# Kernel optimization log

Hardware: AMD Instinct MI355X
Metric: run time of the kernel (lower is better)

The kernel has to match this reference:

```python
import math
import jax, jax.numpy as jnp
import numpy as np

N_HEADS = 16


def setup_inputs() -> dict:
    key = jax.random.key(0)
    k1, k2 = jax.random.split(key)
    qkv = jax.random.normal(k1, (2, 3072, 2048), dtype=jnp.float32)
    mask = jax.random.randint(k2, (2, 1, 2048), 0, 2).astype(jnp.bool_)
    return {"qkv": qkv, "mask": mask}


def reference(qkv, mask):
    bs, width, length = qkv.shape
    ch = width // (3 * N_HEADS)
    q, k, v = jnp.split(qkv, 3, axis=1)  # each [bs, H*C, T]
    scale = 1.0 / math.sqrt(math.sqrt(ch))  # applied to both q and k
    q = (q * scale).reshape(bs * N_HEADS, ch, length)
    k = (k * scale).reshape(bs * N_HEADS, ch, length)
    # [B*H, T, T] scores
    weight = jnp.einsum('bct,bcs->bts', q, k)
    # mask: [bs, 1, T] bool, True = valid token
    inv = ~mask[:, 0, :]                      # [bs, T]
    pad = inv[:, None, :] | inv[:, :, None]   # [bs, T, T]
    pad = jnp.broadcast_to(pad[:, None], (bs, N_HEADS, length, length))
    pad = pad.reshape(bs * N_HEADS, length, length)
    weight = jnp.where(pad, jnp.finfo(weight.dtype).min, weight)
    weight = jax.nn.softmax(weight.astype(jnp.float32), axis=-1).astype(qkv.dtype)
    a = jnp.einsum('bts,bcs->bct', weight, v.reshape(bs * N_HEADS, ch, length))
    return a.reshape(bs, N_HEADS * ch, length)
```

## Files before the change

kernel.cpp:

```cpp
#include <hip/hip_runtime.h>
#include <float.h>


typedef __attribute__((ext_vector_type(8))) short bf16x8;
typedef __attribute__((ext_vector_type(4))) float f32x4;

#define TSEQ 2048
#define QT_OFF 0L
#define KF_OFF 4194304L
#define VF_OFF 8388608L

#if __has_builtin(__builtin_amdgcn_exp2f)
#define EXPFN(x) __builtin_amdgcn_exp2f(x)
#define SM_SCALE (0.125f * 1.44269504088896f)
#else
#define EXPFN(x) __expf(x)
#define SM_SCALE 0.125f
#endif

__device__ inline short f2bf(float x) {
    union { float f; unsigned u; } un; un.f = x;
    unsigned r = un.u + 0x7fffu + ((un.u >> 16) & 1u);
    return (short)(r >> 16);
}

__device__ inline unsigned pkbf(float a, float b) {
    unsigned au = __float_as_uint(a) + 0x8000u;
    unsigned bu = __float_as_uint(b) + 0x8000u;
    return __builtin_amdgcn_perm(bu, au, 0x07060302u);
}

__global__ __launch_bounds__(256) void prep_kernel(
    const float* __restrict__ qkv, short* __restrict__ ws)
{
    const int tid = threadIdx.x;
    const int job = blockIdx.x;
    if (job < 2048) {
        __shared__ float Ls[64 * 65];
        const int which = job & 1;
        const int rest  = job >> 1;
        const int bh = rest & 31, tt = rest >> 5;
        const int b = bh >> 4, h = bh & 15;
        const float* src = qkv + (long)b * 6291456 + ((long)(which * 1024 + h * 64)) * TSEQ + tt * 64;
        #pragma unroll
        for (int ch = 0; ch < 4; ++ch) {
            int idx = tid + ch * 256;
            int c = idx >> 4, tch = idx & 15;
            float4 v = *(const float4*)(src + (long)c * TSEQ + tch * 4);
            float* L = &Ls[c * 65 + tch * 4];
            L[0] = v.x; L[1] = v.y; L[2] = v.z; L[3] = v.w;
        }
        __syncthreads();
        if (which == 0) {
            short* dst = ws + QT_OFF + ((long)bh * TSEQ + tt * 64) * 64;
            #pragma unroll
            for (int ch = 0; ch < 2; ++ch) {
                int idx = tid + ch * 256;
                int t = idx >> 3, cch = idx & 7;
                bf16x8 o;
                #pragma unroll
                for (int j = 0; j < 8; ++j)
                    o[j] = f2bf(Ls[(cch * 8 + j) * 65 + t] * SM_SCALE);
                *(bf16x8*)(dst + (long)t * 64 + cch * 8) = o;
            }
        } else {
            short* dst = ws + KF_OFF + (long)(bh * 32 + tt) * 4096;
            #pragma unroll
            for (int ch = 0; ch < 2; ++ch) {
                int u = tid + ch * 256;
                int f = u >> 6, lane = u & 63;
                int q = lane >> 4, l15 = lane & 15;
                int hf = f & 1, ns = f >> 1;
                bf16x8 o;
                #pragma unroll
                for (int j = 0; j < 8; ++j)
                    o[j] = f2bf(Ls[(hf * 32 + q * 8 + j) * 65 + ns * 16 + l15]);
                *(bf16x8*)(dst + f * 512 + lane * 8) = o;
            }
        }
    } else {
        const int v = job - 2048;
        const int head = v >> 5, it = v & 31;
        const int b = head >> 4, h = head & 15;
        short* dst = ws + VF_OFF + (long)(head * 32 + it) * 4096;
        #pragma unroll
        for (int ch = 0; ch < 2; ++ch) {
            int u = tid * 2 + ch;
            int f = u >> 6, lane = u & 63;
            int q = lane >> 4, l15 = lane & 15;
            int hf = f & 1, nc = f >> 1;
            const float* src = qkv + (long)b * 6291456
                + ((long)(2048 + h * 64 + nc * 16 + l15)) * TSEQ
                + it * 64 + hf * 32 + q * 8;
            float4 a  = *(const float4*)src;
            float4 c4 = *(const float4*)(src + 4);
            bf16x8 o;
            o[0] = f2bf(a.x);  o[1] = f2bf(a.y);  o[2] = f2bf(a.z);  o[3] = f2bf(a.w);
            o[4] = f2bf(c4.x); o[5] = f2bf(c4.y); o[6] = f2bf(c4.z); o[7] = f2bf(c4.w);
            *(bf16x8*)(dst + f * 512 + lane * 8) = o;
        }
    }
}

__global__ __launch_bounds__(512, 2) void attn_kernel(
    const short* __restrict__ ws, const int* __restrict__ mask,
    float* __restrict__ out)
{
    __shared__ __align__(16) char smem[66560];
    short* Ps  = (short*)smem;
    float* mbf = (float*)(smem + 32768);
    float* Os  = (float*)smem;

    const int tid  = threadIdx.x;
    const int lane = tid & 63, wid = tid >> 6;
    const int l15  = lane & 15, quad = lane >> 4;

    const int blk  = blockIdx.x;
    const int head = blk & 31;
    const int qt   = blk >> 5;
    const int b    = head >> 4, h = head & 15;
    const int t0   = qt * 256;

    const short* QT = ws + QT_OFF + (long)head * 131072;
    const short* KF = ws + KF_OFF + (long)head * 131072;
    const short* VF = ws + VF_OFF + (long)head * 131072;
    const long obase = ((long)b * 1024 + h * 64) * TSEQ;

    for (int i = tid; i < TSEQ; i += 512)
        mbf[i] = (mask[b * TSEQ + i] != 0) ? 0.0f : -1e30f;
    __syncthreads();

    bf16x8 qb[2][2];
    #pragma unroll
    for (int nt = 0; nt < 2; ++nt)
        #pragma unroll
        for (int hf = 0; hf < 2; ++hf)
            qb[nt][hf] = *(const bf16x8*)(QT +
                (long)(t0 + wid * 32 + nt * 16 + l15) * 64 + quad * 8 + hf * 32);
    bool qv[2];
    #pragma unroll
    for (int nt = 0; nt < 2; ++nt)
        qv[nt] = (mbf[t0 + wid * 32 + nt * 16 + l15] != 0.0f);

    float l_s[2] = {0.0f, 0.0f};
    f32x4 Oacc[2][4];
    #pragma unroll
    for (int mt = 0; mt < 2; ++mt)
        #pragma unroll
        for (int nc = 0; nc < 4; ++nc)
            #pragma unroll
            for (int r = 0; r < 4; ++r) Oacc[mt][nc][r] = 0.0f;

    short* Pw = Ps + wid * 2048;

    bf16x8 kc[8];
    #pragma unroll
    for (int f = 0; f < 8; ++f)
        kc[f] = *(const bf16x8*)(KF + (long)f * 512 + lane * 8);

    for (int it = 0; it < 32; ++it) {
        const int itn = (it + 1) & 31;

        bf16x8 vf[8];
        #pragma unroll
        for (int f = 0; f < 8; ++f)
            vf[f] = *(const bf16x8*)(VF + ((long)it * 8 + f) * 512 + lane * 8);
        bf16x8 kn[8];
        #pragma unroll
        for (int f = 0; f < 8; ++f)
            kn[f] = *(const bf16x8*)(KF + ((long)itn * 8 + f) * 512 + lane * 8);

        f32x4 bias[4];
        #pragma unroll
        for (int ns = 0; ns < 4; ++ns)
            bias[ns] = *(const f32x4*)&mbf[it * 64 + ns * 16 + quad * 4];

        f32x4 Sacc[4][2];
        #pragma unroll
        for (int ns = 0; ns < 4; ++ns)
            #pragma unroll
            for (int nt = 0; nt < 2; ++nt) {
                Sacc[ns][nt] = __builtin_amdgcn_mfma_f32_16x16x32_bf16(
                    kc[ns * 2 + 0], qb[nt][0], bias[ns], 0, 0, 0);
                Sacc[ns][nt] = __builtin_amdgcn_mfma_f32_16x16x32_bf16(
                    kc[ns * 2 + 1], qb[nt][1], Sacc[ns][nt], 0, 0, 0);
            }

        #pragma unroll
        for (int nt = 0; nt < 2; ++nt) {
            const int row = nt * 16 + l15;
            const int sw  = (row & 7) ^ ((row & 8) >> 1);
            float ls = 0.0f;
            #pragma unroll
            for (int ns = 0; ns < 4; ++ns) {
                float pv[4];
                #pragma unroll
                for (int r = 0; r < 4; ++r) {
                    float e = EXPFN(Sacc[ns][nt][r]);
                    pv[r] = qv[nt] ? 1.0f : e;
                    ls += pv[r];
                }
                const int cbp = (ns * 2 + (quad >> 1)) ^ sw;
                uint2 pk;
                pk.x = pkbf(pv[0], pv[1]);
                pk.y = pkbf(pv[2], pv[3]);
                *(uint2*)&Pw[row * 64 + cbp * 8 + (quad & 1) * 4] = pk;
            }
            ls += __shfl_xor(ls, 16);
            ls += __shfl_xor(ls, 32);
            l_s[nt] += ls;
        }

        bf16x8 pa[2][2];
        #pragma unroll
        for (int mt = 0; mt < 2; ++mt) {
            const int row = mt * 16 + l15;
            const int sw  = (row & 7) ^ ((row & 8) >> 1);
            #pragma unroll
            for (int hf = 0; hf < 2; ++hf)
                pa[mt][hf] = *(const bf16x8*)&Pw[row * 64 + ((quad + 4 * hf) ^ sw) * 8];
        }
        #pragma unroll
        for (int hf = 0; hf < 2; ++hf)
            #pragma unroll
            for (int nc = 0; nc < 4; ++nc)
                #pragma unroll
                for (int mt = 0; mt < 2; ++mt)
                    Oacc[mt][nc] = __builtin_amdgcn_mfma_f32_16x16x32_bf16(
                        pa[mt][hf], vf[nc * 2 + hf], Oacc[mt][nc], 0, 0, 0);

        #pragma unroll
        for (int f = 0; f < 8; ++f) kc[f] = kn[f];
    }

    __syncthreads();
    float inv[2];
    #pragma unroll
    for (int nt = 0; nt < 2; ++nt) inv[nt] = 1.0f / l_s[nt];
    float iw[2][4];
    #pragma unroll
    for (int mt = 0; mt < 2; ++mt)
        #pragma unroll
        for (int r = 0; r < 4; ++r)
            iw[mt][r] = __shfl(inv[mt], 4 * quad + r);
    #pragma unroll
    for (int mt = 0; mt < 2; ++mt)
        #pragma unroll
        for (int nc = 0; nc < 4; ++nc) {
            float4 o;
            o.x = Oacc[mt][nc][0] * iw[mt][0];
            o.y = Oacc[mt][nc][1] * iw[mt][1];
            o.z = Oacc[mt][nc][2] * iw[mt][2];
            o.w = Oacc[mt][nc][3] * iw[mt][3];
            *(float4*)&Os[(nc * 16 + l15) * 260 + wid * 32 + mt * 16 + quad * 4] = o;
        }
    __syncthreads();
    #pragma unroll
    for (int ch = 0; ch < 8; ++ch) {
        int idx = tid + ch * 512;
        int c = idx >> 6, tch = idx & 63;
        *(float4*)(out + obase + (long)c * TSEQ + t0 + tch * 4) =
            *(const float4*)&Os[c * 260 + tch * 4];
    }
}

extern "C" void kernel_launch(void* const* d_in, const int* in_sizes, int n_in,
                              void* d_out, int out_size, void* d_ws, size_t ws_size,
                              hipStream_t stream) {
    const float* qkv  = (const float*)d_in[0];
    const int*   mask = (const int*)d_in[1];
    float*       out  = (float*)d_out;
    short*       ws   = (short*)d_ws;
    prep_kernel<<<dim3(3072), dim3(256), 0, stream>>>(qkv, ws);
    attn_kernel<<<dim3(256), dim3(512), 0, stream>>>(ws, mask, out);
}
```

Measured before the change: 143.2 us.

## Stage K/V tiles through double-buffered LDS via direct global-to-LDS loads

The attention kernel now loads K and V tiles into a double-buffered shared-memory ring using global_load_lds, so each tile is fetched once per block instead of once per wave into registers. Blocks shrink to 256 threads covering 128 query rows, and the grid grows to 512 blocks. The V path in the prep kernel now stages through LDS to make global reads coalesced. The change targets redundant per-wave global traffic and register pressure, at the cost of one block-wide barrier per iteration and twice as many blocks each re-reading K/V.

```diff
diff --git a/kernel.cpp b/kernel.cpp
--- a/kernel.cpp
+++ b/kernel.cpp
@@ -17,6 +17,12 @@
 #define EXPFN(x) __expf(x)
 #define SM_SCALE 0.125f
 #endif
+
+__device__ inline void gload_lds16(const void* g, void* l) {
+    __builtin_amdgcn_global_load_lds(
+        (const __attribute__((address_space(1))) void*)g,
+        (__attribute__((address_space(3))) void*)l, 16, 0, 0);
+}
 
 __device__ inline short f2bf(float x) {
     union { float f; unsigned u; } un; un.f = x;
@@ -68,47 +74,52 @@
             #pragma unroll
             for (int ch = 0; ch < 2; ++ch) {
                 int u = tid + ch * 256;
-                int f = u >> 6, lane = u & 63;
-                int q = lane >> 4, l15 = lane & 15;
+                int f = u >> 6, ln = u & 63;
+                int q = ln >> 4, l = ln & 15;
                 int hf = f & 1, ns = f >> 1;
                 bf16x8 o;
                 #pragma unroll
                 for (int j = 0; j < 8; ++j)
-                    o[j] = f2bf(Ls[(hf * 32 + q * 8 + j) * 65 + ns * 16 + l15]);
-                *(bf16x8*)(dst + f * 512 + lane * 8) = o;
+                    o[j] = f2bf(Ls[(hf * 32 + q * 8 + j) * 65 + ns * 16 + l]);
+                *(bf16x8*)(dst + f * 512 + ln * 8) = o;
             }
         }
     } else {
+        __shared__ float Ls[64 * 68];
         const int v = job - 2048;
         const int head = v >> 5, it = v & 31;
         const int b = head >> 4, h = head & 15;
+        const float* src = qkv + (long)b * 6291456 + ((long)(2048 + h * 64)) * TSEQ + it * 64;
+        const int c = tid >> 2, sq = (tid & 3) * 16;
+        #pragma unroll
+        for (int i = 0; i < 4; ++i) {
+            float4 x = *(const float4*)(src + (long)c * TSEQ + sq + i * 4);
+            *(float4*)&Ls[c * 68 + sq + i * 4] = x;
+        }
+        __syncthreads();
         short* dst = ws + VF_OFF + (long)(head * 32 + it) * 4096;
         #pragma unroll
         for (int ch = 0; ch < 2; ++ch) {
-            int u = tid * 2 + ch;
-            int f = u >> 6, lane = u & 63;
-            int q = lane >> 4, l15 = lane & 15;
+            int u = tid + ch * 256;
+            int f = u >> 6, ln = u & 63;
+            int q = ln >> 4, l = ln & 15;
             int hf = f & 1, nc = f >> 1;
-            const float* src = qkv + (long)b * 6291456
-                + ((long)(2048 + h * 64 + nc * 16 + l15)) * TSEQ
-                + it * 64 + hf * 32 + q * 8;
-            float4 a  = *(const float4*)src;
-            float4 c4 = *(const float4*)(src + 4);
+            const float* Lp = &Ls[(nc * 16 + l) * 68 + hf * 32 + q * 8];
             bf16x8 o;
-            o[0] = f2bf(a.x);  o[1] = f2bf(a.y);  o[2] = f2bf(a.z);  o[3] = f2bf(a.w);
-            o[4] = f2bf(c4.x); o[5] = f2bf(c4.y); o[6] = f2bf(c4.z); o[7] = f2bf(c4.w);
-            *(bf16x8*)(dst + f * 512 + lane * 8) = o;
-        }
-    }
-}
-
-__global__ __launch_bounds__(512, 2) void attn_kernel(
+            #pragma unroll
+            for (int j = 0; j < 8; ++j) o[j] = f2bf(Lp[j]);
+            *(bf16x8*)(dst + f * 512 + ln * 8) = o;
+        }
+    }
+}
+
+__global__ __launch_bounds__(256, 2) void attn_kernel(
     const short* __restrict__ ws, const int* __restrict__ mask,
     float* __restrict__ out)
 {
-    __shared__ __align__(16) char smem[66560];
-    short* Ps  = (short*)smem;
-    float* mbf = (float*)(smem + 32768);
+    __shared__ __align__(16) char smem[57344];
+    short* Ps  = (short*)(smem + 32768);
+    float* mbf = (float*)(smem + 49152);
     float* Os  = (float*)smem;
 
     const int tid  = threadIdx.x;
@@ -119,16 +130,15 @@
     const int head = blk & 31;
     const int qt   = blk >> 5;
     const int b    = head >> 4, h = head & 15;
-    const int t0   = qt * 256;
+    const int t0   = qt * 128;
 
     const short* QT = ws + QT_OFF + (long)head * 131072;
     const short* KF = ws + KF_OFF + (long)head * 131072;
     const short* VF = ws + VF_OFF + (long)head * 131072;
     const long obase = ((long)b * 1024 + h * 64) * TSEQ;
 
-    for (int i = tid; i < TSEQ; i += 512)
+    for (int i = tid; i < TSEQ; i += 256)
         mbf[i] = (mask[b * TSEQ + i] != 0) ? 0.0f : -1e30f;
-    __syncthreads();
 
     bf16x8 qb[2][2];
     #pragma unroll
@@ -137,6 +147,15 @@
         for (int hf = 0; hf < 2; ++hf)
             qb[nt][hf] = *(const bf16x8*)(QT +
                 (long)(t0 + wid * 32 + nt * 16 + l15) * 64 + quad * 8 + hf * 32);
+
+    #pragma unroll
+    for (int i = 0; i < 2; ++i) {
+        int ck = wid * 2 + i;
+        gload_lds16(KF + ck * 512 + lane * 8, smem + ck * 1024);
+        gload_lds16(VF + ck * 512 + lane * 8, smem + 16384 + ck * 1024);
+    }
+    __syncthreads();
+
     bool qv[2];
     #pragma unroll
     for (int nt = 0; nt < 2; ++nt)
@@ -153,22 +172,27 @@
 
     short* Pw = Ps + wid * 2048;
 
-    bf16x8 kc[8];
-    #pragma unroll
-    for (int f = 0; f < 8; ++f)
-        kc[f] = *(const bf16x8*)(KF + (long)f * 512 + lane * 8);
-
     for (int it = 0; it < 32; ++it) {
         const int itn = (it + 1) & 31;
-
-        bf16x8 vf[8];
-        #pragma unroll
-        for (int f = 0; f < 8; ++f)
-            vf[f] = *(const bf16x8*)(VF + ((long)it * 8 + f) * 512 + lane * 8);
-        bf16x8 kn[8];
-        #pragma unroll
-        for (int f = 0; f < 8; ++f)
-            kn[f] = *(const bf16x8*)(KF + ((long)itn * 8 + f) * 512 + lane * 8);
+        const int cur = (it & 1) * 8192;
+        const int nxt = (itn & 1) * 8192;
+
+        #pragma unroll
+        for (int i = 0; i < 2; ++i) {
+            int ck = wid * 2 + i;
+            gload_lds16(KF + (long)itn * 4096 + ck * 512 + lane * 8,
+                        smem + nxt + ck * 1024);
+            gload_lds16(VF + (long)itn * 4096 + ck * 512 + lane * 8,
+                        smem + 16384 + nxt + ck * 1024);
+        }
+
+        const short* Kb = (const short*)(smem + cur);
+        const short* Vb = (const short*)(smem + 16384 + cur);
+        bf16x8 kc[8], vv[8];
+        #pragma unroll
+        for (int f = 0; f < 8; ++f) kc[f] = *(const bf16x8*)(Kb + f * 512 + lane * 8);
+        #pragma unroll
+        for (int f = 0; f < 8; ++f) vv[f] = *(const bf16x8*)(Vb + f * 512 + lane * 8);
 
         f32x4 bias[4];
         #pragma unroll
@@ -227,13 +251,11 @@
                 #pragma unroll
                 for (int mt = 0; mt < 2; ++mt)
                     Oacc[mt][nc] = __builtin_amdgcn_mfma_f32_16x16x32_bf16(
-                        pa[mt][hf], vf[nc * 2 + hf], Oacc[mt][nc], 0, 0, 0);
-
-        #pragma unroll
-        for (int f = 0; f < 8; ++f) kc[f] = kn[f];
-    }
-
-    __syncthreads();
+                        pa[mt][hf], vv[nc * 2 + hf], Oacc[mt][nc], 0, 0, 0);
+
+        __syncthreads();
+    }
+
     float inv[2];
     #pragma unroll
     for (int nt = 0; nt < 2; ++nt) inv[nt] = 1.0f / l_s[nt];
@@ -252,15 +274,15 @@
             o.y = Oacc[mt][nc][1] * iw[mt][1];
             o.z = Oacc[mt][nc][2] * iw[mt][2];
             o.w = Oacc[mt][nc][3] * iw[mt][3];
-            *(float4*)&Os[(nc * 16 + l15) * 260 + wid * 32 + mt * 16 + quad * 4] = o;
+            *(float4*)&Os[(nc * 16 + l15) * 132 + wid * 32 + mt * 16 + quad * 4] = o;
         }
     __syncthreads();
     #pragma unroll
     for (int ch = 0; ch < 8; ++ch) {
-        int idx = tid + ch * 512;
-        int c = idx >> 6, tch = idx & 63;
+        int idx = tid + ch * 256;
+        int c = idx >> 5, tch = idx & 31;
         *(float4*)(out + obase + (long)c * TSEQ + t0 + tch * 4) =
-            *(const float4*)&Os[c * 260 + tch * 4];
+            *(const float4*)&Os[c * 132 + tch * 4];
     }
 }
 
@@ -272,5 +294,5 @@
     float*       out  = (float*)d_out;
     short*       ws   = (short*)d_ws;
     prep_kernel<<<dim3(3072), dim3(256), 0, stream>>>(qkv, ws);
-    attn_kernel<<<dim3(256), dim3(512), 0, stream>>>(ws, mask, out);
-}
+    attn_kernel<<<dim3(512), dim3(256), 0, stream>>>(ws, mask, out);
+}
```

Result: slower. 149.1 us (+4.1%).
